# Kernel tuning notes

Measured on AMD Instinct MI355X. Metric: run time of the kernel, lower is better.

The kernel has to match this reference:

```python
import jax, jax.numpy as jnp
import numpy as np

ALPHA = 0.5


def setup_inputs() -> dict:
    key = jax.random.key(0)
    k1, k2 = jax.random.split(key)
    inputs = jax.random.normal(k1, (16384,), dtype=jnp.float32)
    targets = jax.random.normal(k2, (16384,), dtype=jnp.float32)
    return {"inputs": inputs, "targets": targets}


def reference(inputs, targets):
    # Chamfer 1D: mean over x of min_j |x_i - y_j|, symmetrized with weight alpha.
    x = inputs.reshape(-1)
    y = targets.reshape(-1)
    n = x.shape[0]
    m = y.shape[0]
    # Pairwise absolute differences [N, M]; min over each axis gives both directions.
    d = jnp.abs(x[:, None] - y[None, :])
    cd_xy = jnp.sum(jnp.min(d, axis=1))  # sum_i min_j |x_i - y_j|
    cd_yx = jnp.sum(jnp.min(d, axis=0))  # sum_j min_i |y_j - x_i|
    return ALPHA * cd_xy / n + (1.0 - ALPHA) * cd_yx / m
```

## Files before the change

### kernel.cpp

```cpp
#include <hip/hip_runtime.h>
#include <cfloat>

#define TPB 256
#define BKT 32768
#define SLOTS 16
#define OVCAP 4096
#define RLO -8.0f
#define RSCALE (BKT / 16.0f)
#define ALPHA 0.5f

#define CNT_OFF   0
#define BM1_OFF   (2 * BKT)
#define BM2_OFF   (BM1_OFF + 2048)
#define OVC_OFF   (BM2_OFF + 64)
#define DONE_OFF  (OVC_OFF + 2)
#define ZERO_WORDS (DONE_OFF + 1)
#define SLOTS_OFF (((ZERO_WORDS) + 63) & ~63)
#define OVF_OFF   (SLOTS_OFF + 2 * BKT * SLOTS)

__device__ __forceinline__ int bucket_of(float v) {
    int b = (int)((v - RLO) * RSCALE);
    return min(max(b, 0), BKT - 1);
}

__global__ __launch_bounds__(TPB) void
chamfer_build(const float* __restrict__ x, const float* __restrict__ y,
              int n, int m, unsigned* __restrict__ ws) {
    const int i = blockIdx.x * TPB + threadIdx.x;
    if (i >= n + m) return;
    const bool isx = i < n;
    const int side = isx ? 0 : 1;
    const float v = isx ? x[i] : y[i - n];
    const int b = bucket_of(v);
    const unsigned pos = atomicAdd(ws + CNT_OFF + side * BKT + b, 1u);
    if (pos < SLOTS) {
        ((float*)(ws + SLOTS_OFF))[((size_t)(side * BKT + b)) * SLOTS + pos] = v;
    } else {
        const unsigned o = atomicAdd(ws + OVC_OFF + side, 1u);
        if (o < OVCAP) ((float*)(ws + OVF_OFF))[side * OVCAP + o] = v;
    }
    if (pos == 0) {
        const int W = b >> 5;
        const unsigned old = atomicOr(ws + BM1_OFF + side * 1024 + W, 1u << (b & 31));
        if (old == 0)
            atomicOr(ws + BM2_OFF + side * 32 + (W >> 5), 1u << (W & 31));
    }
}

__device__ __forceinline__ int prev_ne(const unsigned* __restrict__ bm1,
                                       const unsigned* __restrict__ bm2, int b) {
    if (b == 0) return -1;
    const int p = b - 1;
    unsigned w = bm1[p >> 5] & (~0u >> (31 - (p & 31)));
    if (w) return (p & ~31) | (31 - __clz(w));
    const int W = (p >> 5) - 1;
    if (W < 0) return -1;
    int j = W >> 5;
    unsigned w2 = bm2[j] & (~0u >> (31 - (W & 31)));
    while (!w2 && --j >= 0) w2 = bm2[j];
    if (!w2) return -1;
    const int Wp = (j << 5) | (31 - __clz(w2));
    return (Wp << 5) | (31 - __clz(bm1[Wp]));
}
__device__ __forceinline__ int next_ne(const unsigned* __restrict__ bm1,
                                       const unsigned* __restrict__ bm2, int b) {
    if (b >= BKT - 1) return -1;
    const int p = b + 1;
    unsigned w = bm1[p >> 5] & (~0u << (p & 31));
    if (w) return (p & ~31) | (__ffs(w) - 1);
    const int W = (p >> 5) + 1;
    if (W > 1023) return -1;
    int j = W >> 5;
    unsigned w2 = bm2[j] & (~0u << (W & 31));
    while (!w2 && ++j < 32) w2 = bm2[j];
    if (!w2) return -1;
    const int Wp = (j << 5) | (__ffs(w2) - 1);
    return (Wp << 5) | (__ffs(bm1[Wp]) - 1);
}

__device__ __forceinline__ float scan_bucket(const unsigned* __restrict__ cnt,
                                             const float* __restrict__ slots,
                                             int side, int b, float v, float best) {
    const unsigned c = min(cnt[b], (unsigned)SLOTS);
    const float4* sl4 = (const float4*)(slots + ((size_t)(side * BKT + b)) * SLOTS);
    float e[SLOTS];
    *(float4*)(e + 0)  = sl4[0];
    *(float4*)(e + 4)  = sl4[1];
    *(float4*)(e + 8)  = sl4[2];
    *(float4*)(e + 12) = sl4[3];
#pragma unroll
    for (int j = 0; j < SLOTS; ++j) {
        const float d = fabsf(v - e[j]);
        best = ((unsigned)j < c) ? fminf(best, d) : best;
    }
    return best;
}

__global__ __launch_bounds__(TPB) void
chamfer_query(const float* __restrict__ x, const float* __restrict__ y,
              int n, int m, unsigned* __restrict__ ws,
              double* __restrict__ bsums, float* __restrict__ out) {
    const int q = blockIdx.x * TPB + threadIdx.x;
    const int total = n + m;
    double sx = 0.0, sy = 0.0;
    if (q < total) {
        const bool isx = q < n;
        const float v = isx ? x[q] : y[q - n];
        const int side = isx ? 1 : 0;
        const unsigned* cnt = ws + CNT_OFF + side * BKT;
        const unsigned* bm1 = ws + BM1_OFF + side * 1024;
        const unsigned* bm2 = ws + BM2_OFF + side * 32;
        const float* slots = (const float*)(ws + SLOTS_OFF);
        const int b = bucket_of(v);

        float best = scan_bucket(cnt, slots, side, b, v, FLT_MAX);
        const int bp = prev_ne(bm1, bm2, b);
        if (bp >= 0) best = scan_bucket(cnt, slots, side, bp, v, best);
        const int bn = next_ne(bm1, bm2, b);
        if (bn >= 0) best = scan_bucket(cnt, slots, side, bn, v, best);

        const unsigned oc = min(ws[OVC_OFF + side], (unsigned)OVCAP);
        const float* ovf = (const float*)(ws + OVF_OFF) + side * OVCAP;
        for (unsigned k = 0; k < oc; ++k)
            best = fminf(best, fabsf(v - ovf[k]));

        if (isx) sx = (double)best; else sy = (double)best;
    }
    for (int off = 32; off > 0; off >>= 1) {
        sx += __shfl_down(sx, off);
        sy += __shfl_down(sy, off);
    }
    __shared__ double wsx[TPB / 64], wsy[TPB / 64];
    const int w = threadIdx.x >> 6;
    if ((threadIdx.x & 63) == 0) { wsx[w] = sx; wsy[w] = sy; }
    __syncthreads();

    __shared__ bool s_last;
    if (threadIdx.x == 0) {
        double tx = 0.0, ty = 0.0;
#pragma unroll
        for (int i = 0; i < TPB / 64; ++i) { tx += wsx[i]; ty += wsy[i]; }
        bsums[2 * blockIdx.x] = tx;
        bsums[2 * blockIdx.x + 1] = ty;
        __threadfence();
        const unsigned old = atomicAdd(ws + DONE_OFF, 1u);
        s_last = (old == gridDim.x - 1);
    }
    __syncthreads();
    if (!s_last) return;

    __threadfence();
    const int nb = (int)gridDim.x;
    double fx = 0.0, fy = 0.0;
    for (int i = (int)threadIdx.x; i < nb; i += TPB) {
        fx += bsums[2 * i];
        fy += bsums[2 * i + 1];
    }
    for (int off = 32; off > 0; off >>= 1) {
        fx += __shfl_down(fx, off);
        fy += __shfl_down(fy, off);
    }
    __shared__ double lsx[TPB / 64], lsy[TPB / 64];
    const int wave = threadIdx.x >> 6;
    if ((threadIdx.x & 63) == 0) { lsx[wave] = fx; lsy[wave] = fy; }
    __syncthreads();
    if (threadIdx.x == 0) {
        double tx = 0.0, ty = 0.0;
#pragma unroll
        for (int w2 = 0; w2 < TPB / 64; ++w2) { tx += lsx[w2]; ty += lsy[w2]; }
        const double a = (double)ALPHA;
        out[0] = (float)(a * tx / (double)n + (1.0 - a) * ty / (double)m);
    }
}

extern "C" void kernel_launch(void* const* d_in, const int* in_sizes, int n_in,
                              void* d_out, int out_size, void* d_ws, size_t ws_size,
                              hipStream_t stream) {
    const float* x = (const float*)d_in[0];
    const float* y = (const float*)d_in[1];
    const int n = in_sizes[0];
    const int m = in_sizes[1];
    float* out = (float*)d_out;
    const int total = n + m;

    unsigned* ws = (unsigned*)d_ws;
    const size_t meta_bytes = (size_t)(OVF_OFF + 2 * OVCAP) * sizeof(unsigned);
    const size_t meta_al = (meta_bytes + 255) & ~(size_t)255;
    double* bsums = (double*)((char*)d_ws + meta_al);

    const int nb = (total + TPB - 1) / TPB;

    hipMemsetAsync(ws, 0, (size_t)ZERO_WORDS * sizeof(unsigned), stream);
    chamfer_build<<<nb, TPB, 0, stream>>>(x, y, n, m, ws);
    chamfer_query<<<nb, TPB, 0, stream>>>(x, y, n, m, ws, bsums, out);
}
```

Measured before the change: 73.78 us.

## Fuse build and query kernels with a software grid barrier

```diff
diff --git a/kernel.cpp b/kernel.cpp
--- a/kernel.cpp
+++ b/kernel.cpp
@@ -14,7 +14,8 @@
 #define BM2_OFF   (BM1_OFF + 2048)
 #define OVC_OFF   (BM2_OFF + 64)
 #define DONE_OFF  (OVC_OFF + 2)
-#define ZERO_WORDS (DONE_OFF + 1)
+#define ARR_OFF   (DONE_OFF + 1)
+#define ZERO_WORDS (ARR_OFF + 1)
 #define SLOTS_OFF (((ZERO_WORDS) + 63) & ~63)
 #define OVF_OFF   (SLOTS_OFF + 2 * BKT * SLOTS)
 
@@ -23,14 +24,8 @@
     return min(max(b, 0), BKT - 1);
 }
 
-__global__ __launch_bounds__(TPB) void
-chamfer_build(const float* __restrict__ x, const float* __restrict__ y,
-              int n, int m, unsigned* __restrict__ ws) {
-    const int i = blockIdx.x * TPB + threadIdx.x;
-    if (i >= n + m) return;
-    const bool isx = i < n;
-    const int side = isx ? 0 : 1;
-    const float v = isx ? x[i] : y[i - n];
+__device__ __forceinline__ void build_point(float v, int side,
+                                            unsigned* __restrict__ ws) {
     const int b = bucket_of(v);
     const unsigned pos = atomicAdd(ws + CNT_OFF + side * BKT + b, 1u);
     if (pos < SLOTS) {
@@ -96,6 +91,116 @@
     return best;
 }
 
+__device__ __forceinline__ float query_point(float v, int side,
+                                             const unsigned* __restrict__ ws) {
+    const unsigned* cnt = ws + CNT_OFF + side * BKT;
+    const unsigned* bm1 = ws + BM1_OFF + side * 1024;
+    const unsigned* bm2 = ws + BM2_OFF + side * 32;
+    const float* slots = (const float*)(ws + SLOTS_OFF);
+    const int b = bucket_of(v);
+
+    float best = scan_bucket(cnt, slots, side, b, v, FLT_MAX);
+    const int bp = prev_ne(bm1, bm2, b);
+    if (bp >= 0) best = scan_bucket(cnt, slots, side, bp, v, best);
+    const int bn = next_ne(bm1, bm2, b);
+    if (bn >= 0) best = scan_bucket(cnt, slots, side, bn, v, best);
+
+    const unsigned oc = min(ws[OVC_OFF + side], (unsigned)OVCAP);
+    const float* ovf = (const float*)(ws + OVF_OFF) + side * OVCAP;
+    for (unsigned k = 0; k < oc; ++k)
+        best = fminf(best, fabsf(v - ovf[k]));
+    return best;
+}
+
+__global__ __launch_bounds__(TPB) void
+chamfer_fused(const float* __restrict__ x, const float* __restrict__ y,
+              int n, int m, unsigned* __restrict__ ws,
+              double* __restrict__ bsums, float* __restrict__ out) {
+    const int tid = blockIdx.x * TPB + (int)threadIdx.x;
+    const int total = n + m;
+    const unsigned nb = gridDim.x;
+
+    const bool live = tid < total;
+    const bool isx = live && (tid < n);
+    float v = 0.0f;
+    if (live) {
+        v = isx ? x[tid] : y[tid - n];
+        build_point(v, isx ? 0 : 1, ws);
+    }
+
+    __syncthreads();
+    if (threadIdx.x == 0) {
+        __threadfence();
+        atomicAdd(ws + ARR_OFF, 1u);
+        while (__hip_atomic_load(ws + ARR_OFF, __ATOMIC_RELAXED,
+                                 __HIP_MEMORY_SCOPE_AGENT) < nb) {
+            __builtin_amdgcn_s_sleep(1);
+        }
+    }
+    __syncthreads();
+    __threadfence();
+
+    double sx = 0.0, sy = 0.0;
+    if (live) {
+        const float best = query_point(v, isx ? 1 : 0, ws);
+        if (isx) sx = (double)best; else sy = (double)best;
+    }
+    for (int off = 32; off > 0; off >>= 1) {
+        sx += __shfl_down(sx, off);
+        sy += __shfl_down(sy, off);
+    }
+    __shared__ double wsx[TPB / 64], wsy[TPB / 64];
+    const int w = threadIdx.x >> 6;
+    if ((threadIdx.x & 63) == 0) { wsx[w] = sx; wsy[w] = sy; }
+    __syncthreads();
+
+    __shared__ bool s_last;
+    if (threadIdx.x == 0) {
+        double tx = 0.0, ty = 0.0;
+#pragma unroll
+        for (int i = 0; i < TPB / 64; ++i) { tx += wsx[i]; ty += wsy[i]; }
+        bsums[2 * blockIdx.x] = tx;
+        bsums[2 * blockIdx.x + 1] = ty;
+        __threadfence();
+        const unsigned old = atomicAdd(ws + DONE_OFF, 1u);
+        s_last = (old == nb - 1);
+    }
+    __syncthreads();
+    if (!s_last) return;
+
+    __threadfence();
+    double fx = 0.0, fy = 0.0;
+    for (int i = (int)threadIdx.x; i < (int)nb; i += TPB) {
+        fx += bsums[2 * i];
+        fy += bsums[2 * i + 1];
+    }
+    for (int off = 32; off > 0; off >>= 1) {
+        fx += __shfl_down(fx, off);
+        fy += __shfl_down(fy, off);
+    }
+    __shared__ double lsx[TPB / 64], lsy[TPB / 64];
+    const int wave = threadIdx.x >> 6;
+    if ((threadIdx.x & 63) == 0) { lsx[wave] = fx; lsy[wave] = fy; }
+    __syncthreads();
+    if (threadIdx.x == 0) {
+        double tx = 0.0, ty = 0.0;
+#pragma unroll
+        for (int w2 = 0; w2 < TPB / 64; ++w2) { tx += lsx[w2]; ty += lsy[w2]; }
+        const double a = (double)ALPHA;
+        out[0] = (float)(a * tx / (double)n + (1.0 - a) * ty / (double)m);
+    }
+}
+
+__global__ __launch_bounds__(TPB) void
+chamfer_build(const float* __restrict__ x, const float* __restrict__ y,
+              int n, int m, unsigned* __restrict__ ws) {
+    const int i = blockIdx.x * TPB + threadIdx.x;
+    if (i >= n + m) return;
+    const bool isx = i < n;
+    const float v = isx ? x[i] : y[i - n];
+    build_point(v, isx ? 0 : 1, ws);
+}
+
 __global__ __launch_bounds__(TPB) void
 chamfer_query(const float* __restrict__ x, const float* __restrict__ y,
               int n, int m, unsigned* __restrict__ ws,
@@ -106,24 +211,7 @@
     if (q < total) {
         const bool isx = q < n;
         const float v = isx ? x[q] : y[q - n];
-        const int side = isx ? 1 : 0;
-        const unsigned* cnt = ws + CNT_OFF + side * BKT;
-        const unsigned* bm1 = ws + BM1_OFF + side * 1024;
-        const unsigned* bm2 = ws + BM2_OFF + side * 32;
-        const float* slots = (const float*)(ws + SLOTS_OFF);
-        const int b = bucket_of(v);
-
-        float best = scan_bucket(cnt, slots, side, b, v, FLT_MAX);
-        const int bp = prev_ne(bm1, bm2, b);
-        if (bp >= 0) best = scan_bucket(cnt, slots, side, bp, v, best);
-        const int bn = next_ne(bm1, bm2, b);
-        if (bn >= 0) best = scan_bucket(cnt, slots, side, bn, v, best);
-
-        const unsigned oc = min(ws[OVC_OFF + side], (unsigned)OVCAP);
-        const float* ovf = (const float*)(ws + OVF_OFF) + side * OVCAP;
-        for (unsigned k = 0; k < oc; ++k)
-            best = fminf(best, fabsf(v - ovf[k]));
-
+        const float best = query_point(v, isx ? 1 : 0, ws);
         if (isx) sx = (double)best; else sy = (double)best;
     }
     for (int off = 32; off > 0; off >>= 1) {
@@ -134,7 +222,6 @@
     const int w = threadIdx.x >> 6;
     if ((threadIdx.x & 63) == 0) { wsx[w] = sx; wsy[w] = sy; }
     __syncthreads();
-
     __shared__ bool s_last;
     if (threadIdx.x == 0) {
         double tx = 0.0, ty = 0.0;
@@ -148,7 +235,6 @@
     }
     __syncthreads();
     if (!s_last) return;
-
     __threadfence();
     const int nb = (int)gridDim.x;
     double fx = 0.0, fy = 0.0;
@@ -166,7 +252,6 @@
     __syncthreads();
     if (threadIdx.x == 0) {
         double tx = 0.0, ty = 0.0;
-#pragma unroll
         for (int w2 = 0; w2 < TPB / 64; ++w2) { tx += lsx[w2]; ty += lsy[w2]; }
         const double a = (double)ALPHA;
         out[0] = (float)(a * tx / (double)n + (1.0 - a) * ty / (double)m);
@@ -191,6 +276,10 @@
     const int nb = (total + TPB - 1) / TPB;
 
     hipMemsetAsync(ws, 0, (size_t)ZERO_WORDS * sizeof(unsigned), stream);
-    chamfer_build<<<nb, TPB, 0, stream>>>(x, y, n, m, ws);
-    chamfer_query<<<nb, TPB, 0, stream>>>(x, y, n, m, ws, bsums, out);
-}
+    if (nb <= 256) {
+        chamfer_fused<<<nb, TPB, 0, stream>>>(x, y, n, m, ws, bsums, out);
+    } else {
+        chamfer_build<<<nb, TPB, 0, stream>>>(x, y, n, m, ws);
+        chamfer_query<<<nb, TPB, 0, stream>>>(x, y, n, m, ws, bsums, out);
+    }
+}
```

Result: slower. 84.14 us (+14.0%).

## Partition bucket build across blocks with shared-memory counters, drop memset

Applied to the files above, without the earlier changes.

```diff
diff --git a/kernel.cpp b/kernel.cpp
--- a/kernel.cpp
+++ b/kernel.cpp
@@ -2,21 +2,24 @@
 #include <cfloat>
 
 #define TPB 256
+#define NBLK 128
 #define BKT 32768
+#define GBT (2 * BKT)
+#define GB (GBT / NBLK)
 #define SLOTS 16
-#define OVCAP 4096
 #define RLO -8.0f
 #define RSCALE (BKT / 16.0f)
 #define ALPHA 0.5f
 
+static_assert(2 * NBLK == TPB, "ovfc staging assumes one entry per query thread");
+
 #define CNT_OFF   0
-#define BM1_OFF   (2 * BKT)
-#define BM2_OFF   (BM1_OFF + 2048)
-#define OVC_OFF   (BM2_OFF + 64)
-#define DONE_OFF  (OVC_OFF + 2)
-#define ZERO_WORDS (DONE_OFF + 1)
-#define SLOTS_OFF (((ZERO_WORDS) + 63) & ~63)
-#define OVF_OFF   (SLOTS_OFF + 2 * BKT * SLOTS)
+#define BM1_OFF   (GBT)
+#define BM2H_OFF  (BM1_OFF + GBT / 32)
+#define OVFC_OFF  (BM2H_OFF + NBLK)
+#define DONE_OFF  (OVFC_OFF + 2 * NBLK)
+#define SLOTS_OFF (((DONE_OFF + 1) + 15) & ~15)
+#define OVF_OFF   (SLOTS_OFF + GBT * SLOTS)
 
 __device__ __forceinline__ int bucket_of(float v) {
     int b = (int)((v - RLO) * RSCALE);
@@ -26,29 +29,78 @@
 __global__ __launch_bounds__(TPB) void
 chamfer_build(const float* __restrict__ x, const float* __restrict__ y,
               int n, int m, unsigned* __restrict__ ws) {
-    const int i = blockIdx.x * TPB + threadIdx.x;
-    if (i >= n + m) return;
-    const bool isx = i < n;
-    const int side = isx ? 0 : 1;
-    const float v = isx ? x[i] : y[i - n];
-    const int b = bucket_of(v);
-    const unsigned pos = atomicAdd(ws + CNT_OFF + side * BKT + b, 1u);
-    if (pos < SLOTS) {
-        ((float*)(ws + SLOTS_OFF))[((size_t)(side * BKT + b)) * SLOTS + pos] = v;
-    } else {
-        const unsigned o = atomicAdd(ws + OVC_OFF + side, 1u);
-        if (o < OVCAP) ((float*)(ws + OVF_OFF))[side * OVCAP + o] = v;
-    }
-    if (pos == 0) {
-        const int W = b >> 5;
-        const unsigned old = atomicOr(ws + BM1_OFF + side * 1024 + W, 1u << (b & 31));
-        if (old == 0)
-            atomicOr(ws + BM2_OFF + side * 32 + (W >> 5), 1u << (W & 31));
-    }
-}
-
-__device__ __forceinline__ int prev_ne(const unsigned* __restrict__ bm1,
-                                       const unsigned* __restrict__ bm2, int b) {
+    __shared__ unsigned lcnt[GB];
+    __shared__ unsigned lbm1[GB / 32];
+    __shared__ unsigned lovf[2];
+    const int k = blockIdx.x;
+    const int base = k * GB;
+    const int total = n + m;
+    float* const slots = (float*)(ws + SLOTS_OFF);
+    float* const ovf0 = (float*)(ws + OVF_OFF) + (size_t)(2 * k + 0) * total;
+    float* const ovf1 = (float*)(ws + OVF_OFF) + (size_t)(2 * k + 1) * total;
+
+    for (int i = threadIdx.x; i < GB; i += TPB) lcnt[i] = 0;
+    if (threadIdx.x < 2) lovf[threadIdx.x] = 0;
+    if (k == 0 && threadIdx.x == 0) ws[DONE_OFF] = 0;
+    __syncthreads();
+
+    auto catch_elem = [&](float v, int side, float* ovfp) {
+        const int lb = side * BKT + bucket_of(v) - base;
+        if ((unsigned)lb < (unsigned)GB) {
+            const unsigned pos = atomicAdd(&lcnt[lb], 1u);
+            if (pos < SLOTS)
+                slots[(size_t)(base + lb) * SLOTS + pos] = v;
+            else
+                ovfp[atomicAdd(&lovf[side], 1u)] = v;
+        }
+    };
+    {
+        const int n4 = n >> 2;
+        const float4* x4 = (const float4*)x;
+        for (int i = threadIdx.x; i < n4; i += TPB) {
+            const float4 a = x4[i];
+            catch_elem(a.x, 0, ovf0); catch_elem(a.y, 0, ovf0);
+            catch_elem(a.z, 0, ovf0); catch_elem(a.w, 0, ovf0);
+        }
+        for (int i = (n4 << 2) + threadIdx.x; i < n; i += TPB)
+            catch_elem(x[i], 0, ovf0);
+    }
+    {
+        const int m4 = m >> 2;
+        const float4* y4 = (const float4*)y;
+        for (int i = threadIdx.x; i < m4; i += TPB) {
+            const float4 a = y4[i];
+            catch_elem(a.x, 1, ovf1); catch_elem(a.y, 1, ovf1);
+            catch_elem(a.z, 1, ovf1); catch_elem(a.w, 1, ovf1);
+        }
+        for (int i = (m4 << 2) + threadIdx.x; i < m; i += TPB)
+            catch_elem(y[i], 1, ovf1);
+    }
+    __syncthreads();
+
+    for (int i = threadIdx.x; i < GB; i += TPB) ws[CNT_OFF + base + i] = lcnt[i];
+    if (threadIdx.x < GB / 32) {
+        const int w = threadIdx.x;
+        unsigned bits = 0;
+#pragma unroll
+        for (int j = 0; j < 32; ++j)
+            if (lcnt[w * 32 + j]) bits |= 1u << j;
+        lbm1[w] = bits;
+        ws[BM1_OFF + (base >> 5) + w] = bits;
+    }
+    if (threadIdx.x < 2) ws[OVFC_OFF + 2 * k + threadIdx.x] = lovf[threadIdx.x];
+    __syncthreads();
+    if (threadIdx.x == 0) {
+        unsigned bits = 0;
+#pragma unroll
+        for (int w = 0; w < GB / 32; ++w)
+            if (lbm1[w]) bits |= 1u << w;
+        ws[BM2H_OFF + k] = bits << ((k & 1) << 4);
+    }
+}
+
+__device__ __forceinline__ int prev_ne(const unsigned* bm1, const unsigned* bm2,
+                                       int b) {
     if (b == 0) return -1;
     const int p = b - 1;
     unsigned w = bm1[p >> 5] & (~0u >> (31 - (p & 31)));
@@ -62,8 +114,8 @@
     const int Wp = (j << 5) | (31 - __clz(w2));
     return (Wp << 5) | (31 - __clz(bm1[Wp]));
 }
-__device__ __forceinline__ int next_ne(const unsigned* __restrict__ bm1,
-                                       const unsigned* __restrict__ bm2, int b) {
+__device__ __forceinline__ int next_ne(const unsigned* bm1, const unsigned* bm2,
+                                       int b) {
     if (b >= BKT - 1) return -1;
     const int p = b + 1;
     unsigned w = bm1[p >> 5] & (~0u << (p & 31));
@@ -80,9 +132,9 @@
 
 __device__ __forceinline__ float scan_bucket(const unsigned* __restrict__ cnt,
                                              const float* __restrict__ slots,
-                                             int side, int b, float v, float best) {
-    const unsigned c = min(cnt[b], (unsigned)SLOTS);
-    const float4* sl4 = (const float4*)(slots + ((size_t)(side * BKT + b)) * SLOTS);
+                                             int gb, float v, float best) {
+    const unsigned c = min(cnt[gb], (unsigned)SLOTS);
+    const float4* sl4 = (const float4*)(slots + (size_t)gb * SLOTS);
     float e[SLOTS];
     *(float4*)(e + 0)  = sl4[0];
     *(float4*)(e + 4)  = sl4[1];
@@ -100,30 +152,50 @@
 chamfer_query(const float* __restrict__ x, const float* __restrict__ y,
               int n, int m, unsigned* __restrict__ ws,
               double* __restrict__ bsums, float* __restrict__ out) {
-    const int q = blockIdx.x * TPB + threadIdx.x;
+    __shared__ unsigned s_bm1[GBT / 32];
+    __shared__ unsigned s_bm2[64];
+    __shared__ unsigned s_ovfc[2 * NBLK];
+    __shared__ unsigned s_has_ovf;
+
+    const int lt = (int)threadIdx.x;
+    for (int i = lt; i < GBT / 32; i += TPB) s_bm1[i] = ws[BM1_OFF + i];
+    if (lt < 64) s_bm2[lt] = ws[BM2H_OFF + 2 * lt] | ws[BM2H_OFF + 2 * lt + 1];
+    s_ovfc[lt] = ws[OVFC_OFF + lt];
+    if (lt == 0) s_has_ovf = 0;
+    __syncthreads();
+    if (s_ovfc[lt]) atomicOr(&s_has_ovf, 1u);
+    __syncthreads();
+
+    const int q = blockIdx.x * TPB + lt;
     const int total = n + m;
     double sx = 0.0, sy = 0.0;
     if (q < total) {
         const bool isx = q < n;
         const float v = isx ? x[q] : y[q - n];
         const int side = isx ? 1 : 0;
-        const unsigned* cnt = ws + CNT_OFF + side * BKT;
-        const unsigned* bm1 = ws + BM1_OFF + side * 1024;
-        const unsigned* bm2 = ws + BM2_OFF + side * 32;
+        const unsigned* cnt = ws + CNT_OFF;
+        const unsigned* bm1 = s_bm1 + side * (BKT / 32);
+        const unsigned* bm2 = s_bm2 + side * 32;
         const float* slots = (const float*)(ws + SLOTS_OFF);
         const int b = bucket_of(v);
 
-        float best = scan_bucket(cnt, slots, side, b, v, FLT_MAX);
+        float best = scan_bucket(cnt, slots, side * BKT + b, v, FLT_MAX);
         const int bp = prev_ne(bm1, bm2, b);
-        if (bp >= 0) best = scan_bucket(cnt, slots, side, bp, v, best);
+        if (bp >= 0) best = scan_bucket(cnt, slots, side * BKT + bp, v, best);
         const int bn = next_ne(bm1, bm2, b);
-        if (bn >= 0) best = scan_bucket(cnt, slots, side, bn, v, best);
-
-        const unsigned oc = min(ws[OVC_OFF + side], (unsigned)OVCAP);
-        const float* ovf = (const float*)(ws + OVF_OFF) + side * OVCAP;
-        for (unsigned k = 0; k < oc; ++k)
-            best = fminf(best, fabsf(v - ovf[k]));
-
+        if (bn >= 0) best = scan_bucket(cnt, slots, side * BKT + bn, v, best);
+
+        if (s_has_ovf) {
+            const float* ovfbase = (const float*)(ws + OVF_OFF);
+            for (int e = side; e < 2 * NBLK; e += 2) {
+                const unsigned c = s_ovfc[e];
+                if (c) {
+                    const float* op = ovfbase + (size_t)e * total;
+                    for (unsigned j = 0; j < c; ++j)
+                        best = fminf(best, fabsf(v - op[j]));
+                }
+            }
+        }
         if (isx) sx = (double)best; else sy = (double)best;
     }
     for (int off = 32; off > 0; off >>= 1) {
@@ -131,12 +203,12 @@
         sy += __shfl_down(sy, off);
     }
     __shared__ double wsx[TPB / 64], wsy[TPB / 64];
-    const int w = threadIdx.x >> 6;
-    if ((threadIdx.x & 63) == 0) { wsx[w] = sx; wsy[w] = sy; }
+    const int w = lt >> 6;
+    if ((lt & 63) == 0) { wsx[w] = sx; wsy[w] = sy; }
     __syncthreads();
 
     __shared__ bool s_last;
-    if (threadIdx.x == 0) {
+    if (lt == 0) {
         double tx = 0.0, ty = 0.0;
 #pragma unroll
         for (int i = 0; i < TPB / 64; ++i) { tx += wsx[i]; ty += wsy[i]; }
@@ -152,7 +224,7 @@
     __threadfence();
     const int nb = (int)gridDim.x;
     double fx = 0.0, fy = 0.0;
-    for (int i = (int)threadIdx.x; i < nb; i += TPB) {
+    for (int i = lt; i < nb; i += TPB) {
         fx += bsums[2 * i];
         fy += bsums[2 * i + 1];
     }
@@ -161,10 +233,10 @@
         fy += __shfl_down(fy, off);
     }
     __shared__ double lsx[TPB / 64], lsy[TPB / 64];
-    const int wave = threadIdx.x >> 6;
-    if ((threadIdx.x & 63) == 0) { lsx[wave] = fx; lsy[wave] = fy; }
-    __syncthreads();
-    if (threadIdx.x == 0) {
+    const int wave = lt >> 6;
+    if ((lt & 63) == 0) { lsx[wave] = fx; lsy[wave] = fy; }
+    __syncthreads();
+    if (lt == 0) {
         double tx = 0.0, ty = 0.0;
 #pragma unroll
         for (int w2 = 0; w2 < TPB / 64; ++w2) { tx += lsx[w2]; ty += lsy[w2]; }
@@ -184,13 +256,13 @@
     const int total = n + m;
 
     unsigned* ws = (unsigned*)d_ws;
-    const size_t meta_bytes = (size_t)(OVF_OFF + 2 * OVCAP) * sizeof(unsigned);
+    const size_t ovf_words = (size_t)2 * NBLK * total;
+    const size_t meta_bytes = (size_t)(OVF_OFF + ovf_words) * sizeof(unsigned);
     const size_t meta_al = (meta_bytes + 255) & ~(size_t)255;
     double* bsums = (double*)((char*)d_ws + meta_al);
 
-    const int nb = (total + TPB - 1) / TPB;
-
-    hipMemsetAsync(ws, 0, (size_t)ZERO_WORDS * sizeof(unsigned), stream);
-    chamfer_build<<<nb, TPB, 0, stream>>>(x, y, n, m, ws);
-    chamfer_query<<<nb, TPB, 0, stream>>>(x, y, n, m, ws, bsums, out);
-}
+    const int nbq = (total + TPB - 1) / TPB;
+
+    chamfer_build<<<NBLK, TPB, 0, stream>>>(x, y, n, m, ws);
+    chamfer_query<<<nbq, TPB, 0, stream>>>(x, y, n, m, ws, bsums, out);
+}
```

New measurement: 80.18 us. 1.09x slower.
